# Performance work log

Hardware: AMD Instinct MI355X
Metric: run time of the kernel (lower is better)

The kernel has to match this reference:

```python
import jax, jax.numpy as jnp
import numpy as np

DIM = 1024
HEADS = 16
HEAD_DIM = DIM // HEADS
HIDDEN = 4 * DIM
EPS = 1e-5

def _layernorm(x, w, b):
    mu = jnp.mean(x, axis=-1, keepdims=True)
    var = jnp.mean(jnp.square(x - mu), axis=-1, keepdims=True)
    return (x - mu) * jax.lax.rsqrt(var + EPS) * w + b

def setup_inputs() -> dict:
    key = jax.random.key(0)
    ks = jax.random.split(key, 8)
    B, N, C = 4, 1024, DIM
    s = lambda fan_in: 1.0 / np.sqrt(fan_in)
    return {
        "x": jax.random.normal(ks[0], (B, N, C), dtype=jnp.float32),
        "ln1_w": jnp.ones((C,), jnp.float32),
        "ln1_b": jnp.zeros((C,), jnp.float32),
        "qkv_w": jax.random.normal(ks[1], (3 * C, C), jnp.float32) * s(C),
        "proj_w": jax.random.normal(ks[2], (C, C), jnp.float32) * s(C),
        "proj_b": jnp.zeros((C,), jnp.float32),
        "ln2_w": jnp.ones((C,), jnp.float32),
        "ln2_b": jnp.zeros((C,), jnp.float32),
        "fc1_w": jax.random.normal(ks[3], (HIDDEN, C), jnp.float32) * s(C),
        "fc1_b": jnp.zeros((HIDDEN,), jnp.float32),
        "fc2_w": jax.random.normal(ks[4], (C, HIDDEN), jnp.float32) * s(HIDDEN),
        "fc2_b": jnp.zeros((C,), jnp.float32),
    }

def reference(x, ln1_w, ln1_b, qkv_w, proj_w, proj_b, ln2_w, ln2_b, fc1_w, fc1_b, fc2_w, fc2_b):
    B, N, C = x.shape
    H, D = HEADS, HEAD_DIM
    scale = D ** -0.5
    # --- attention branch (pre-norm) ---
    h = _layernorm(x, ln1_w, ln1_b)
    qkv = jnp.einsum('bnc,oc->bno', h, qkv_w)          # [B,N,3C], no bias (qkv_bias=False)
    qkv = qkv.reshape(B, N, 3, H, D)
    q = jnp.transpose(qkv[:, :, 0], (0, 2, 1, 3))       # [B,H,N,D]
    k = jnp.transpose(qkv[:, :, 1], (0, 2, 1, 3))
    v = jnp.transpose(qkv[:, :, 2], (0, 2, 1, 3))
    attn = jnp.einsum('bhnd,bhmd->bhnm', q, k) * scale  # [B,H,N,N]
    attn = jax.nn.softmax(attn, axis=-1)
    o = jnp.einsum('bhnm,bhmd->bhnd', attn, v)          # [B,H,N,D]
    o = jnp.transpose(o, (0, 2, 1, 3)).reshape(B, N, C)
    o = jnp.einsum('bnc,oc->bno', o, proj_w) + proj_b
    x = x + o
    # --- MLP branch (pre-norm); drop=0.0 -> identity ---
    h = _layernorm(x, ln2_w, ln2_b)
    h = jnp.einsum('bnc,hc->bnh', h, fc1_w) + fc1_b
    h = jax.nn.gelu(h, approximate=False)               # nn.GELU exact erf form
    h = jnp.einsum('bnh,ch->bnc', h, fc2_w) + fc2_b
    return x + h
```

## Files before the change

### kernel.cpp

```cpp
#include <hip/hip_runtime.h>
#include <hip/hip_bf16.h>
#include <math.h>
#include <stdint.h>

#define SEQ 1024
#define CDIM 1024
#define NHEAD 16
#define HIDDEN 4096
#define BATCH 4
#define MROWS (BATCH*SEQ)

using bf16x8 = __attribute__((ext_vector_type(8))) short;
using f32x4  = __attribute__((ext_vector_type(4))) float;

__device__ __forceinline__ short f2bf(float f) {
    union { float f; uint32_t u; } c; c.f = f;
    const uint32_t u = c.u + 0x7FFFu + ((c.u >> 16) & 1u);
    return (short)(u >> 16);
}

__device__ __forceinline__ float gelu_exact(float v) {
    return 0.5f * v * (1.0f + erff(v * 0.70710678118654752440f));
}

__device__ __forceinline__ void gload_lds16(const short* g, short* lds) {
    __builtin_amdgcn_global_load_lds(
        (const __attribute__((address_space(1))) void*)(uintptr_t)g,
        (__attribute__((address_space(3))) void*)(uintptr_t)lds,
        16, 0, 0);
}

__global__ void cvt_bf16_kernel(const float* __restrict__ in, short* __restrict__ out) {
    const size_t i = ((size_t)blockIdx.x * 256 + threadIdx.x) * 8;
    const float4 a = *(const float4*)(in + i);
    const float4 b = *(const float4*)(in + i + 4);
    bf16x8 s;
    s[0] = f2bf(a.x); s[1] = f2bf(a.y); s[2] = f2bf(a.z); s[3] = f2bf(a.w);
    s[4] = f2bf(b.x); s[5] = f2bf(b.y); s[6] = f2bf(b.z); s[7] = f2bf(b.w);
    *(bf16x8*)(out + i) = s;
}

__global__ void ln_kernel(const float* __restrict__ x, const float* __restrict__ w,
                          const float* __restrict__ b, short* __restrict__ out) {
    const int row = blockIdx.x;
    const int t = threadIdx.x;
    const float4* xr = (const float4*)(x + (size_t)row * CDIM);
    float4 v = xr[t];
    float s  = v.x + v.y + v.z + v.w;
    float sq = v.x*v.x + v.y*v.y + v.z*v.z + v.w*v.w;
    #pragma unroll
    for (int off = 32; off; off >>= 1) {
        s  += __shfl_down(s, off);
        sq += __shfl_down(sq, off);
    }
    __shared__ float ss[4], ssq[4];
    const int wid = t >> 6, lane = t & 63;
    if (lane == 0) { ss[wid] = s; ssq[wid] = sq; }
    __syncthreads();
    s  = ss[0] + ss[1] + ss[2] + ss[3];
    sq = ssq[0] + ssq[1] + ssq[2] + ssq[3];
    const float mu  = s * (1.0f / CDIM);
    const float var = sq * (1.0f / CDIM) - mu * mu;
    const float rs  = rsqrtf(var + 1e-5f);
    const float4 wv = ((const float4*)w)[t];
    const float4 bv = ((const float4*)b)[t];
    short4 o;
    o.x = f2bf((v.x - mu) * rs * wv.x + bv.x);
    o.y = f2bf((v.y - mu) * rs * wv.y + bv.y);
    o.z = f2bf((v.z - mu) * rs * wv.z + bv.z);
    o.w = f2bf((v.w - mu) * rs * wv.w + bv.w);
    *(short4*)(out + (size_t)row * CDIM + t * 4) = o;
}

template<int BN, bool BIAS, bool RES, bool GELU_, bool OUTBF16>
__global__ __launch_bounds__(256) void mgemm(
    const short* __restrict__ A, const short* __restrict__ B,
    const float* __restrict__ bias, const float* __restrict__ res,
    void* __restrict__ Cv, int M, int N, int K)
{
    constexpr int MF = (BN == 128) ? 4 : 2;
    __shared__ __align__(16) short As[3][128 * 32];
    __shared__ __align__(16) short Bs[3][BN * 32];
    const int t = threadIdx.x;
    const int w = t >> 6, l = t & 63;

    const int gx = gridDim.x;
    const int nwg = gx * gridDim.y;
    const int lid = blockIdx.y * gx + blockIdx.x;
    const int swz = (lid & 7) * (nwg >> 3) + (lid >> 3);
    const int bx = swz % gx, by = swz / gx;
    const int m0 = by * 128, n0 = bx * BN;

    const int wrow = (BN == 128) ? (w >> 1) * 64 : w * 32;
    const int wcol = (BN == 128) ? (w & 1) * 64 : 0;

    const short* agp0 = A + (size_t)(m0 + w * 32 + (l >> 2)) * K + (l & 3) * 8;
    const short* agp1 = agp0 + (size_t)16 * K;
    const short* bgp0;
    const short* bgp1 = nullptr;
    if (BN == 128) {
        bgp0 = B + (size_t)(n0 + w * 32 + (l >> 2)) * K + (l & 3) * 8;
        bgp1 = bgp0 + (size_t)16 * K;
    } else {
        bgp0 = B + (size_t)(n0 + w * 16 + (l >> 2)) * K + (l & 3) * 8;
    }

    int aoff[MF], boff[4];
    #pragma unroll
    for (int m = 0; m < MF; ++m) aoff[m] = (wrow + m * 16 + (l & 15)) * 32 + (l >> 4) * 8;
    #pragma unroll
    for (int n = 0; n < 4; ++n)  boff[n] = (wcol + n * 16 + (l & 15)) * 32 + (l >> 4) * 8;

    auto stage = [&](int k0, int buf) {
        short* ldsA = &As[buf][w * 1024];
        gload_lds16(agp0 + k0, ldsA);
        gload_lds16(agp1 + k0, ldsA + 512);
        if (BN == 128) {
            short* ldsB = &Bs[buf][w * 1024];
            gload_lds16(bgp0 + k0, ldsB);
            gload_lds16(bgp1 + k0, ldsB + 512);
        } else {
            gload_lds16(bgp0 + k0, &Bs[buf][w * 512]);
        }
    };

    f32x4 acc[MF][4] = {};
    const int T = K / 32;
    stage(0, 0);
    stage(32, 1);
    int cur = 0;
    for (int kt = 0; kt < T; ++kt) {
        if (kt < T - 1) {
            if constexpr (BN == 128) asm volatile("s_waitcnt vmcnt(4)" ::: "memory");
            else                     asm volatile("s_waitcnt vmcnt(3)" ::: "memory");
        } else {
            asm volatile("s_waitcnt vmcnt(0)" ::: "memory");
        }
        __builtin_amdgcn_sched_barrier(0);
        __builtin_amdgcn_s_barrier();
        __builtin_amdgcn_sched_barrier(0);
        if (kt + 2 < T) {
            int nb = kt + 2; nb -= (nb >= 3) ? ((nb / 3) * 3) : 0;
            stage((kt + 2) * 32, nb);
        }
        bf16x8 af[MF], bfr[4];
        #pragma unroll
        for (int m = 0; m < MF; ++m) af[m]  = *(const bf16x8*)&As[cur][aoff[m]];
        #pragma unroll
        for (int n = 0; n < 4; ++n)  bfr[n] = *(const bf16x8*)&Bs[cur][boff[n]];
        #pragma unroll
        for (int m = 0; m < MF; ++m)
            #pragma unroll
            for (int n = 0; n < 4; ++n)
                acc[m][n] = __builtin_amdgcn_mfma_f32_16x16x32_bf16(af[m], bfr[n], acc[m][n], 0, 0, 0);
        cur = (cur == 2) ? 0 : cur + 1;
    }

    const int lr4 = (l >> 4) * 4, lc = l & 15;
    #pragma unroll
    for (int m = 0; m < MF; ++m) {
        #pragma unroll
        for (int n = 0; n < 4; ++n) {
            const int col = n0 + wcol + n * 16 + lc;
            const float bv = BIAS ? bias[col] : 0.0f;
            #pragma unroll
            for (int r = 0; r < 4; ++r) {
                const int row = m0 + wrow + m * 16 + lr4 + r;
                float v = acc[m][n][r] + bv;
                if (GELU_) v = gelu_exact(v);
                if (RES)   v += res[(size_t)row * N + col];
                if (OUTBF16) ((short*)Cv)[(size_t)row * N + col] = f2bf(v);
                else         ((float*)Cv)[(size_t)row * N + col] = v;
            }
        }
    }
}

__global__ __launch_bounds__(256) void qkv_gemm(
    const short* __restrict__ A, const short* __restrict__ B,
    short* __restrict__ qkvb, short* __restrict__ VT, int K)
{
    __shared__ __align__(16) short As[3][128 * 32];
    __shared__ __align__(16) short Bs[3][128 * 32];
    const int t = threadIdx.x;
    const int w = t >> 6, l = t & 63;
    const int wr = w >> 1, wc = w & 1;

    const int gx = gridDim.x;
    const int nwg = gx * gridDim.y;
    const int lid = blockIdx.y * gx + blockIdx.x;
    const int swz = (lid & 7) * (nwg >> 3) + (lid >> 3);
    const int bx = swz % gx, by = swz / gx;
    const int m0 = by * 128, n0 = bx * 128;

    const short* agp0 = A + (size_t)(m0 + w * 32 + (l >> 2)) * K + (l & 3) * 8;
    const short* agp1 = agp0 + (size_t)16 * K;
    const short* bgp0 = B + (size_t)(n0 + w * 32 + (l >> 2)) * K + (l & 3) * 8;
    const short* bgp1 = bgp0 + (size_t)16 * K;

    int aoff[4], boff[4];
    #pragma unroll
    for (int m = 0; m < 4; ++m) aoff[m] = (wr * 64 + m * 16 + (l & 15)) * 32 + (l >> 4) * 8;
    #pragma unroll
    for (int n = 0; n < 4; ++n) boff[n] = (wc * 64 + n * 16 + (l & 15)) * 32 + (l >> 4) * 8;

    auto stage = [&](int k0, int buf) {
        short* ldsA = &As[buf][w * 1024];
        short* ldsB = &Bs[buf][w * 1024];
        gload_lds16(agp0 + k0, ldsA);
        gload_lds16(agp1 + k0, ldsA + 512);
        gload_lds16(bgp0 + k0, ldsB);
        gload_lds16(bgp1 + k0, ldsB + 512);
    };

    f32x4 acc[4][4] = {};
    const int T = K / 32;
    stage(0, 0);
    stage(32, 1);
    int cur = 0;
    for (int kt = 0; kt < T; ++kt) {
        if (kt < T - 1) asm volatile("s_waitcnt vmcnt(4)" ::: "memory");
        else            asm volatile("s_waitcnt vmcnt(0)" ::: "memory");
        __builtin_amdgcn_sched_barrier(0);
        __builtin_amdgcn_s_barrier();
        __builtin_amdgcn_sched_barrier(0);
        if (kt + 2 < T) {
            int nb = kt + 2; nb -= (nb >= 3) ? ((nb / 3) * 3) : 0;
            stage((kt + 2) * 32, nb);
        }
        bf16x8 af[4], bfr[4];
        #pragma unroll
        for (int m = 0; m < 4; ++m) af[m]  = *(const bf16x8*)&As[cur][aoff[m]];
        #pragma unroll
        for (int n = 0; n < 4; ++n) bfr[n] = *(const bf16x8*)&Bs[cur][boff[n]];
        #pragma unroll
        for (int m = 0; m < 4; ++m)
            #pragma unroll
            for (int n = 0; n < 4; ++n)
                acc[m][n] = __builtin_amdgcn_mfma_f32_16x16x32_bf16(af[m], bfr[n], acc[m][n], 0, 0, 0);
        cur = (cur == 2) ? 0 : cur + 1;
    }

    const int lr4 = (l >> 4) * 4, lc = l & 15;
    if (n0 < 2048) {
        const float sc = (n0 < 1024) ? 0.125f : 1.0f;
        #pragma unroll
        for (int m = 0; m < 4; ++m) {
            #pragma unroll
            for (int n = 0; n < 4; ++n) {
                const int col = n0 + wc * 64 + n * 16 + lc;
                #pragma unroll
                for (int r = 0; r < 4; ++r) {
                    const int row = m0 + wr * 64 + m * 16 + lr4 + r;
                    qkvb[(size_t)row * 2048 + col] = f2bf(acc[m][n][r] * sc);
                }
            }
        }
    } else {
        #pragma unroll
        for (int m = 0; m < 4; ++m) {
            const int row0 = m0 + wr * 64 + m * 16 + lr4;
            const int b = row0 >> 10, nseq = row0 & 1023;
            #pragma unroll
            for (int n = 0; n < 4; ++n) {
                const int c2 = n0 - 2048 + wc * 64 + n * 16 + lc;
                const int h = c2 >> 6, d = c2 & 63;
                short4 v4;
                v4.x = f2bf(acc[m][n][0]); v4.y = f2bf(acc[m][n][1]);
                v4.z = f2bf(acc[m][n][2]); v4.w = f2bf(acc[m][n][3]);
                *(short4*)&VT[(((size_t)(b * 16 + h) * 64 + d) * 1024) + nseq] = v4;
            }
        }
    }
}

__global__ __launch_bounds__(256) void fattn(const short* __restrict__ qkvb,
                                             const short* __restrict__ VT,
                                             short* __restrict__ o) {
    const int bh = blockIdx.y;
    const int b = bh >> 4, h = bh & 15;
    const int q0 = blockIdx.x * 64;
    const int t = threadIdx.x, w = t >> 6, l = t & 63;

    __shared__ __align__(16) short Ks[2][64 * 64];
    __shared__ __align__(16) short Vs[2][64 * 64];
    __shared__ __align__(16) short Ps[4][1024];

    const size_t qrow = (size_t)(b * SEQ + q0 + w * 16 + (l & 15)) * 2048 + h * 64;
    bf16x8 qf[2];
    qf[0] = *(const bf16x8*)&qkvb[qrow + (l >> 4) * 8];
    qf[1] = *(const bf16x8*)&qkvb[qrow + 32 + (l >> 4) * 8];

    const int srow = l >> 3;
    const int sc16 = (l & 7) ^ (srow & 7);
    const short* Kg = qkvb + 1024 + h * 64;
    const short* Vg = VT + (size_t)bh * 64 * 1024;

    f32x4 acc[4] = {};
    float mrow[4] = {-1e30f, -1e30f, -1e30f, -1e30f};
    float lrow[4] = {0.f, 0.f, 0.f, 0.f};

    auto stage = [&](int kt, int buf) {
        const int kv0 = kt * 64;
        #pragma unroll
        for (int i = 0; i < 2; ++i) {
            const int r0 = w * 16 + i * 8;
            gload_lds16(Kg + (size_t)(b * SEQ + kv0 + r0 + srow) * 2048 + sc16 * 8,
                        &Ks[buf][r0 * 64]);
            gload_lds16(Vg + (size_t)(r0 + srow) * 1024 + kv0 + sc16 * 8,
                        &Vs[buf][r0 * 64]);
        }
    };

    stage(0, 0);
    for (int kt = 0; kt < 16; ++kt) {
        const int cur = kt & 1;
        __syncthreads();
        if (kt + 1 < 16) stage(kt + 1, cur ^ 1);

        f32x4 sacc[4];
        #pragma unroll
        for (int nt = 0; nt < 4; ++nt) {
            f32x4 z = {};
            #pragma unroll
            for (int ks = 0; ks < 2; ++ks) {
                const int row = nt * 16 + (l & 15);
                const int c16 = (ks * 4 + (l >> 4)) ^ (row & 7);
                const bf16x8 kf = *(const bf16x8*)&Ks[cur][row * 64 + c16 * 8];
                z = __builtin_amdgcn_mfma_f32_16x16x32_bf16(qf[ks], kf, z, 0, 0, 0);
            }
            sacc[nt] = z;
        }
        float tmax[4], tsum[4], fac[4];
        #pragma unroll
        for (int r = 0; r < 4; ++r)
            tmax[r] = fmaxf(fmaxf(sacc[0][r], sacc[1][r]), fmaxf(sacc[2][r], sacc[3][r]));
        #pragma unroll
        for (int off = 1; off <= 8; off <<= 1)
            #pragma unroll
            for (int r = 0; r < 4; ++r)
                tmax[r] = fmaxf(tmax[r], __shfl_xor(tmax[r], off));
        #pragma unroll
        for (int r = 0; r < 4; ++r) {
            const float nm = fmaxf(mrow[r], tmax[r]);
            fac[r] = __expf(mrow[r] - nm);
            mrow[r] = nm;
            tsum[r] = 0.0f;
        }
        #pragma unroll
        for (int nt = 0; nt < 4; ++nt) {
            #pragma unroll
            for (int r = 0; r < 4; ++r) {
                const float p = __expf(sacc[nt][r] - mrow[r]);
                tsum[r] += p;
                const int q = (l >> 4) * 4 + r;
                const int kv = nt * 16 + (l & 15);
                union { float f; uint32_t u; } cu; cu.f = p;
                Ps[w][q * 64 + (kv ^ ((q & 7) << 3))] = (short)((cu.u + 0x8000u) >> 16);
            }
        }
        #pragma unroll
        for (int off = 1; off <= 8; off <<= 1)
            #pragma unroll
            for (int r = 0; r < 4; ++r)
                tsum[r] += __shfl_xor(tsum[r], off);
        #pragma unroll
        for (int r = 0; r < 4; ++r) lrow[r] = lrow[r] * fac[r] + tsum[r];
        #pragma unroll
        for (int nt2 = 0; nt2 < 4; ++nt2)
            #pragma unroll
            for (int r = 0; r < 4; ++r)
                acc[nt2][r] *= fac[r];
        #pragma unroll
        for (int ks = 0; ks < 2; ++ks) {
            const int ql = l & 15;
            const bf16x8 pa = *(const bf16x8*)&Ps[w][ql * 64 + ((ks * 32 + (l >> 4) * 8) ^ ((ql & 7) << 3))];
            #pragma unroll
            for (int nt2 = 0; nt2 < 4; ++nt2) {
                const int row = nt2 * 16 + (l & 15);
                const int c16 = (ks * 4 + (l >> 4)) ^ (row & 7);
                const bf16x8 vf = *(const bf16x8*)&Vs[cur][row * 64 + c16 * 8];
                acc[nt2] = __builtin_amdgcn_mfma_f32_16x16x32_bf16(pa, vf, acc[nt2], 0, 0, 0);
            }
        }
    }
    #pragma unroll
    for (int r = 0; r < 4; ++r) {
        const float rcp = 1.0f / lrow[r];
        const int q = q0 + w * 16 + (l >> 4) * 4 + r;
        #pragma unroll
        for (int nt2 = 0; nt2 < 4; ++nt2) {
            const int d = nt2 * 16 + (l & 15);
            o[(size_t)(b * SEQ + q) * CDIM + h * 64 + d] = f2bf(acc[nt2][r] * rcp);
        }
    }
}

extern "C" void kernel_launch(void* const* d_in, const int* in_sizes, int n_in,
                              void* d_out, int out_size, void* d_ws, size_t ws_size,
                              hipStream_t stream) {
    const float* x      = (const float*)d_in[0];
    const float* ln1_w  = (const float*)d_in[1];
    const float* ln1_b  = (const float*)d_in[2];
    const float* qkv_w  = (const float*)d_in[3];
    const float* proj_w = (const float*)d_in[4];
    const float* proj_b = (const float*)d_in[5];
    const float* ln2_w  = (const float*)d_in[6];
    const float* ln2_b  = (const float*)d_in[7];
    const float* fc1_w  = (const float*)d_in[8];
    const float* fc1_b  = (const float*)d_in[9];
    const float* fc2_w  = (const float*)d_in[10];
    const float* fc2_b  = (const float*)d_in[11];
    float* out = (float*)d_out;

    short* ws16  = (short*)d_ws;
    short* wqkv  = ws16;
    short* wproj = ws16 + 3145728;
    short* wfc1  = ws16 + 4194304;
    short* wfc2  = ws16 + 8388608;
    char*  wsb   = (char*)d_ws;
    short* qkvb  = (short*)(wsb + (size_t)24 * 1024 * 1024);
    short* VT    = (short*)(wsb + (size_t)40 * 1024 * 1024);
    short* mlp1  = (short*)(wsb + (size_t)24 * 1024 * 1024);
    short* hbuf  = (short*)(wsb + (size_t)72 * 1024 * 1024);

    cvt_bf16_kernel<<<1536, 256, 0, stream>>>(qkv_w, wqkv);
    cvt_bf16_kernel<<< 512, 256, 0, stream>>>(proj_w, wproj);
    cvt_bf16_kernel<<<2048, 256, 0, stream>>>(fc1_w, wfc1);
    cvt_bf16_kernel<<<2048, 256, 0, stream>>>(fc2_w, wfc2);

    ln_kernel<<<MROWS, 256, 0, stream>>>(x, ln1_w, ln1_b, hbuf);
    qkv_gemm<<<dim3(24, 32), 256, 0, stream>>>(hbuf, wqkv, qkvb, VT, 1024);
    fattn<<<dim3(SEQ / 64, BATCH * NHEAD), 256, 0, stream>>>(qkvb, VT, hbuf);
    mgemm<64,true,true,false,false><<<dim3(16, 32), 256, 0, stream>>>(
        hbuf, wproj, proj_b, x, out, MROWS, 1024, 1024);
    ln_kernel<<<MROWS, 256, 0, stream>>>(out, ln2_w, ln2_b, hbuf);
    mgemm<128,true,false,true,true><<<dim3(32, 32), 256, 0, stream>>>(
        hbuf, wfc1, fc1_b, nullptr, mlp1, MROWS, 4096, 1024);
    mgemm<64,true,true,false,false><<<dim3(16, 32), 256, 0, stream>>>(
        mlp1, wfc2, fc2_b, out, out, MROWS, 1024, 4096);
}
```

Measured before the change: 252.1 us.

## Swizzle GEMM LDS layout, retile proj/fc2, restructure flash softmax, fuse weight casts

Fuses the four weight-conversion launches into one kernel. Adds an XOR swizzle to the GEMM LDS staging and fragment reads to avoid bank conflicts. Retiles the proj and fc2 GEMMs from 128x64 to 64x128 blocks with a 2x2 wave layout. In attention it swaps the MFMA operands so each lane holds one query row, uses lazy rescaling that skips the max update unless it grows past a threshold, packs P to bf16 with a hardware convert, and remaps blocks so heads share the cache. Several independent changes add risk in correctness and in register pressure.

```diff
diff --git a/kernel.cpp b/kernel.cpp
--- a/kernel.cpp
+++ b/kernel.cpp
@@ -30,8 +30,17 @@
         16, 0, 0);
 }
 
-__global__ void cvt_bf16_kernel(const float* __restrict__ in, short* __restrict__ out) {
-    const size_t i = ((size_t)blockIdx.x * 256 + threadIdx.x) * 8;
+__global__ void cvt_all_kernel(const float* __restrict__ qkv_w, const float* __restrict__ proj_w,
+                               const float* __restrict__ fc1_w, const float* __restrict__ fc2_w,
+                               short* __restrict__ wq, short* __restrict__ wp,
+                               short* __restrict__ w1, short* __restrict__ w2) {
+    const int blk = blockIdx.x;
+    const float* in; short* out; size_t base;
+    if (blk < 1536)      { in = qkv_w;  out = wq; base = (size_t)blk * 2048; }
+    else if (blk < 2048) { in = proj_w; out = wp; base = (size_t)(blk - 1536) * 2048; }
+    else if (blk < 4096) { in = fc1_w;  out = w1; base = (size_t)(blk - 2048) * 2048; }
+    else                 { in = fc2_w;  out = w2; base = (size_t)(blk - 4096) * 2048; }
+    const size_t i = base + (size_t)threadIdx.x * 8;
     const float4 a = *(const float4*)(in + i);
     const float4 b = *(const float4*)(in + i + 4);
     bf16x8 s;
@@ -72,14 +81,17 @@
     *(short4*)(out + (size_t)row * CDIM + t * 4) = o;
 }
 
-template<int BN, bool BIAS, bool RES, bool GELU_, bool OUTBF16>
+template<int BM, int BN, bool BIAS, bool RES, bool GELU_, bool OUTBF16>
 __global__ __launch_bounds__(256) void mgemm(
     const short* __restrict__ A, const short* __restrict__ B,
     const float* __restrict__ bias, const float* __restrict__ res,
     void* __restrict__ Cv, int M, int N, int K)
 {
-    constexpr int MF = (BN == 128) ? 4 : 2;
-    __shared__ __align__(16) short As[3][128 * 32];
+    constexpr int MF = BM / 32;
+    constexpr int NF = BN / 32;
+    constexpr int CA = BM / 64;
+    constexpr int CB = BN / 64;
+    __shared__ __align__(16) short As[3][BM * 32];
     __shared__ __align__(16) short Bs[3][BN * 32];
     const int t = threadIdx.x;
     const int w = t >> 6, l = t & 63;
@@ -87,52 +99,43 @@
     const int gx = gridDim.x;
     const int nwg = gx * gridDim.y;
     const int lid = blockIdx.y * gx + blockIdx.x;
-    const int swz = (lid & 7) * (nwg >> 3) + (lid >> 3);
-    const int bx = swz % gx, by = swz / gx;
-    const int m0 = by * 128, n0 = bx * BN;
-
-    const int wrow = (BN == 128) ? (w >> 1) * 64 : w * 32;
-    const int wcol = (BN == 128) ? (w & 1) * 64 : 0;
-
-    const short* agp0 = A + (size_t)(m0 + w * 32 + (l >> 2)) * K + (l & 3) * 8;
-    const short* agp1 = agp0 + (size_t)16 * K;
-    const short* bgp0;
-    const short* bgp1 = nullptr;
-    if (BN == 128) {
-        bgp0 = B + (size_t)(n0 + w * 32 + (l >> 2)) * K + (l & 3) * 8;
-        bgp1 = bgp0 + (size_t)16 * K;
-    } else {
-        bgp0 = B + (size_t)(n0 + w * 16 + (l >> 2)) * K + (l & 3) * 8;
-    }
-
-    int aoff[MF], boff[4];
-    #pragma unroll
-    for (int m = 0; m < MF; ++m) aoff[m] = (wrow + m * 16 + (l & 15)) * 32 + (l >> 4) * 8;
-    #pragma unroll
-    for (int n = 0; n < 4; ++n)  boff[n] = (wcol + n * 16 + (l & 15)) * 32 + (l >> 4) * 8;
+    const int swzb = (lid & 7) * (nwg >> 3) + (lid >> 3);
+    const int bx = swzb % gx, by = swzb / gx;
+    const int m0 = by * BM, n0 = bx * BN;
+
+    const int wrow = (w >> 1) * (BM / 2);
+    const int wcol = (w & 1) * (BN / 2);
+
+    const int sk8 = ((l & 3) ^ ((l >> 3) & 3)) * 8;
+    const short* agp = A + (size_t)(m0 + w * 16 * CA + (l >> 2)) * K + sk8;
+    const short* bgp = B + (size_t)(n0 + w * 16 * CB + (l >> 2)) * K + sk8;
+
+    const int fr = l & 15;
+    const int rk = ((l >> 4) ^ ((fr >> 1) & 3)) * 8;
+    int aoff[MF], boff[NF];
+    #pragma unroll
+    for (int m = 0; m < MF; ++m) aoff[m] = (wrow + m * 16 + fr) * 32 + rk;
+    #pragma unroll
+    for (int n = 0; n < NF; ++n) boff[n] = (wcol + n * 16 + fr) * 32 + rk;
 
     auto stage = [&](int k0, int buf) {
-        short* ldsA = &As[buf][w * 1024];
-        gload_lds16(agp0 + k0, ldsA);
-        gload_lds16(agp1 + k0, ldsA + 512);
-        if (BN == 128) {
-            short* ldsB = &Bs[buf][w * 1024];
-            gload_lds16(bgp0 + k0, ldsB);
-            gload_lds16(bgp1 + k0, ldsB + 512);
-        } else {
-            gload_lds16(bgp0 + k0, &Bs[buf][w * 512]);
-        }
+        #pragma unroll
+        for (int c = 0; c < CA; ++c)
+            gload_lds16(agp + (size_t)(c * 16) * K + k0, &As[buf][(w * CA + c) * 512]);
+        #pragma unroll
+        for (int c = 0; c < CB; ++c)
+            gload_lds16(bgp + (size_t)(c * 16) * K + k0, &Bs[buf][(w * CB + c) * 512]);
     };
 
-    f32x4 acc[MF][4] = {};
+    f32x4 acc[MF][NF] = {};
     const int T = K / 32;
     stage(0, 0);
     stage(32, 1);
     int cur = 0;
     for (int kt = 0; kt < T; ++kt) {
         if (kt < T - 1) {
-            if constexpr (BN == 128) asm volatile("s_waitcnt vmcnt(4)" ::: "memory");
-            else                     asm volatile("s_waitcnt vmcnt(3)" ::: "memory");
+            if constexpr (CA + CB == 4) asm volatile("s_waitcnt vmcnt(4)" ::: "memory");
+            else                        asm volatile("s_waitcnt vmcnt(3)" ::: "memory");
         } else {
             asm volatile("s_waitcnt vmcnt(0)" ::: "memory");
         }
@@ -143,15 +146,15 @@
             int nb = kt + 2; nb -= (nb >= 3) ? ((nb / 3) * 3) : 0;
             stage((kt + 2) * 32, nb);
         }
-        bf16x8 af[MF], bfr[4];
+        bf16x8 af[MF], bfr[NF];
         #pragma unroll
         for (int m = 0; m < MF; ++m) af[m]  = *(const bf16x8*)&As[cur][aoff[m]];
         #pragma unroll
-        for (int n = 0; n < 4; ++n)  bfr[n] = *(const bf16x8*)&Bs[cur][boff[n]];
+        for (int n = 0; n < NF; ++n) bfr[n] = *(const bf16x8*)&Bs[cur][boff[n]];
         #pragma unroll
         for (int m = 0; m < MF; ++m)
             #pragma unroll
-            for (int n = 0; n < 4; ++n)
+            for (int n = 0; n < NF; ++n)
                 acc[m][n] = __builtin_amdgcn_mfma_f32_16x16x32_bf16(af[m], bfr[n], acc[m][n], 0, 0, 0);
         cur = (cur == 2) ? 0 : cur + 1;
     }
@@ -160,7 +163,7 @@
     #pragma unroll
     for (int m = 0; m < MF; ++m) {
         #pragma unroll
-        for (int n = 0; n < 4; ++n) {
+        for (int n = 0; n < NF; ++n) {
             const int col = n0 + wcol + n * 16 + lc;
             const float bv = BIAS ? bias[col] : 0.0f;
             #pragma unroll
@@ -176,7 +179,7 @@
     }
 }
 
-__global__ __launch_bounds__(256) void qkv_gemm(
+__global__ __launch_bounds__(256) void qkv_m(
     const short* __restrict__ A, const short* __restrict__ B,
     short* __restrict__ qkvb, short* __restrict__ VT, int K)
 {
@@ -184,33 +187,36 @@
     __shared__ __align__(16) short Bs[3][128 * 32];
     const int t = threadIdx.x;
     const int w = t >> 6, l = t & 63;
-    const int wr = w >> 1, wc = w & 1;
 
     const int gx = gridDim.x;
     const int nwg = gx * gridDim.y;
     const int lid = blockIdx.y * gx + blockIdx.x;
-    const int swz = (lid & 7) * (nwg >> 3) + (lid >> 3);
-    const int bx = swz % gx, by = swz / gx;
+    const int swzb = (lid & 7) * (nwg >> 3) + (lid >> 3);
+    const int bx = swzb % gx, by = swzb / gx;
     const int m0 = by * 128, n0 = bx * 128;
 
-    const short* agp0 = A + (size_t)(m0 + w * 32 + (l >> 2)) * K + (l & 3) * 8;
-    const short* agp1 = agp0 + (size_t)16 * K;
-    const short* bgp0 = B + (size_t)(n0 + w * 32 + (l >> 2)) * K + (l & 3) * 8;
-    const short* bgp1 = bgp0 + (size_t)16 * K;
-
+    const int wrow = (w >> 1) * 64;
+    const int wcol = (w & 1) * 64;
+
+    const int sk8 = ((l & 3) ^ ((l >> 3) & 3)) * 8;
+    const short* agp = A + (size_t)(m0 + w * 32 + (l >> 2)) * K + sk8;
+    const short* bgp = B + (size_t)(n0 + w * 32 + (l >> 2)) * K + sk8;
+
+    const int fr = l & 15;
+    const int rk = ((l >> 4) ^ ((fr >> 1) & 3)) * 8;
     int aoff[4], boff[4];
     #pragma unroll
-    for (int m = 0; m < 4; ++m) aoff[m] = (wr * 64 + m * 16 + (l & 15)) * 32 + (l >> 4) * 8;
-    #pragma unroll
-    for (int n = 0; n < 4; ++n) boff[n] = (wc * 64 + n * 16 + (l & 15)) * 32 + (l >> 4) * 8;
+    for (int m = 0; m < 4; ++m) aoff[m] = (wrow + m * 16 + fr) * 32 + rk;
+    #pragma unroll
+    for (int n = 0; n < 4; ++n) boff[n] = (wcol + n * 16 + fr) * 32 + rk;
 
     auto stage = [&](int k0, int buf) {
-        short* ldsA = &As[buf][w * 1024];
-        short* ldsB = &Bs[buf][w * 1024];
-        gload_lds16(agp0 + k0, ldsA);
-        gload_lds16(agp1 + k0, ldsA + 512);
-        gload_lds16(bgp0 + k0, ldsB);
-        gload_lds16(bgp1 + k0, ldsB + 512);
+        #pragma unroll
+        for (int c = 0; c < 2; ++c)
+            gload_lds16(agp + (size_t)(c * 16) * K + k0, &As[buf][(w * 2 + c) * 512]);
+        #pragma unroll
+        for (int c = 0; c < 2; ++c)
+            gload_lds16(bgp + (size_t)(c * 16) * K + k0, &Bs[buf][(w * 2 + c) * 512]);
     };
 
     f32x4 acc[4][4] = {};
@@ -248,10 +254,10 @@
         for (int m = 0; m < 4; ++m) {
             #pragma unroll
             for (int n = 0; n < 4; ++n) {
-                const int col = n0 + wc * 64 + n * 16 + lc;
+                const int col = n0 + wcol + n * 16 + lc;
                 #pragma unroll
                 for (int r = 0; r < 4; ++r) {
-                    const int row = m0 + wr * 64 + m * 16 + lr4 + r;
+                    const int row = m0 + wrow + m * 16 + lr4 + r;
                     qkvb[(size_t)row * 2048 + col] = f2bf(acc[m][n][r] * sc);
                 }
             }
@@ -259,11 +265,11 @@
     } else {
         #pragma unroll
         for (int m = 0; m < 4; ++m) {
-            const int row0 = m0 + wr * 64 + m * 16 + lr4;
+            const int row0 = m0 + wrow + m * 16 + lr4;
             const int b = row0 >> 10, nseq = row0 & 1023;
             #pragma unroll
             for (int n = 0; n < 4; ++n) {
-                const int c2 = n0 - 2048 + wc * 64 + n * 16 + lc;
+                const int c2 = n0 - 2048 + wcol + n * 16 + lc;
                 const int h = c2 >> 6, d = c2 & 63;
                 short4 v4;
                 v4.x = f2bf(acc[m][n][0]); v4.y = f2bf(acc[m][n][1]);
@@ -277,9 +283,10 @@
 __global__ __launch_bounds__(256) void fattn(const short* __restrict__ qkvb,
                                              const short* __restrict__ VT,
                                              short* __restrict__ o) {
-    const int bh = blockIdx.y;
+    const int lid = blockIdx.y * gridDim.x + blockIdx.x;
+    const int bh = ((lid >> 7) << 3) | (lid & 7);
+    const int q0 = ((lid >> 3) & 15) * 64;
     const int b = bh >> 4, h = bh & 15;
-    const int q0 = blockIdx.x * 64;
     const int t = threadIdx.x, w = t >> 6, l = t & 63;
 
     __shared__ __align__(16) short Ks[2][64 * 64];
@@ -297,8 +304,9 @@
     const short* Vg = VT + (size_t)bh * 64 * 1024;
 
     f32x4 acc[4] = {};
-    float mrow[4] = {-1e30f, -1e30f, -1e30f, -1e30f};
-    float lrow[4] = {0.f, 0.f, 0.f, 0.f};
+    float mr = -1e30f, lr = 0.0f;
+    const int q = l & 15;
+    const int g4 = (l >> 4) & 3;
 
     auto stage = [&](int kt, int buf) {
         const int kv0 = kt * 64;
@@ -327,50 +335,57 @@
                 const int row = nt * 16 + (l & 15);
                 const int c16 = (ks * 4 + (l >> 4)) ^ (row & 7);
                 const bf16x8 kf = *(const bf16x8*)&Ks[cur][row * 64 + c16 * 8];
-                z = __builtin_amdgcn_mfma_f32_16x16x32_bf16(qf[ks], kf, z, 0, 0, 0);
+                z = __builtin_amdgcn_mfma_f32_16x16x32_bf16(kf, qf[ks], z, 0, 0, 0);
             }
             sacc[nt] = z;
         }
-        float tmax[4], tsum[4], fac[4];
-        #pragma unroll
-        for (int r = 0; r < 4; ++r)
-            tmax[r] = fmaxf(fmaxf(sacc[0][r], sacc[1][r]), fmaxf(sacc[2][r], sacc[3][r]));
-        #pragma unroll
-        for (int off = 1; off <= 8; off <<= 1)
+        float tm = sacc[0][0];
+        #pragma unroll
+        for (int nt = 0; nt < 4; ++nt)
+            #pragma unroll
+            for (int r = 0; r < 4; ++r) tm = fmaxf(tm, sacc[nt][r]);
+        tm = fmaxf(tm, __shfl_xor(tm, 16));
+        tm = fmaxf(tm, __shfl_xor(tm, 32));
+        const bool norescale = __all(tm <= mr + 8.0f);
+        float fac = 1.0f;
+        if (!norescale) {
+            const float nm = fmaxf(mr, tm);
+            fac = __expf(mr - nm);
+            mr = nm;
+        }
+        float p[4][4];
+        float ts = 0.0f;
+        #pragma unroll
+        for (int nt = 0; nt < 4; ++nt)
+            #pragma unroll
+            for (int r = 0; r < 4; ++r) {
+                p[nt][r] = __expf(sacc[nt][r] - mr);
+                ts += p[nt][r];
+            }
+        ts += __shfl_xor(ts, 16);
+        ts += __shfl_xor(ts, 32);
+        lr = lr * fac + ts;
+        if (!norescale) {
+            float facv[4];
             #pragma unroll
             for (int r = 0; r < 4; ++r)
-                tmax[r] = fmaxf(tmax[r], __shfl_xor(tmax[r], off));
-        #pragma unroll
-        for (int r = 0; r < 4; ++r) {
-            const float nm = fmaxf(mrow[r], tmax[r]);
-            fac[r] = __expf(mrow[r] - nm);
-            mrow[r] = nm;
-            tsum[r] = 0.0f;
+                facv[r] = __shfl(fac, (l & 48) + g4 * 4 + r);
+            #pragma unroll
+            for (int nt2 = 0; nt2 < 4; ++nt2)
+                #pragma unroll
+                for (int r = 0; r < 4; ++r)
+                    acc[nt2][r] *= facv[r];
         }
         #pragma unroll
         for (int nt = 0; nt < 4; ++nt) {
-            #pragma unroll
-            for (int r = 0; r < 4; ++r) {
-                const float p = __expf(sacc[nt][r] - mrow[r]);
-                tsum[r] += p;
-                const int q = (l >> 4) * 4 + r;
-                const int kv = nt * 16 + (l & 15);
-                union { float f; uint32_t u; } cu; cu.f = p;
-                Ps[w][q * 64 + (kv ^ ((q & 7) << 3))] = (short)((cu.u + 0x8000u) >> 16);
-            }
-        }
-        #pragma unroll
-        for (int off = 1; off <= 8; off <<= 1)
-            #pragma unroll
-            for (int r = 0; r < 4; ++r)
-                tsum[r] += __shfl_xor(tsum[r], off);
-        #pragma unroll
-        for (int r = 0; r < 4; ++r) lrow[r] = lrow[r] * fac[r] + tsum[r];
-        #pragma unroll
-        for (int nt2 = 0; nt2 < 4; ++nt2)
-            #pragma unroll
-            for (int r = 0; r < 4; ++r)
-                acc[nt2][r] *= fac[r];
+            uint32_t lo, hi;
+            asm("v_cvt_pk_bf16_f32 %0, %1, %2" : "=v"(lo) : "v"(p[nt][0]), "v"(p[nt][1]));
+            asm("v_cvt_pk_bf16_f32 %0, %1, %2" : "=v"(hi) : "v"(p[nt][2]), "v"(p[nt][3]));
+            const int kvb = nt * 16 + g4 * 4;
+            const int addr = q * 64 + (((kvb >> 3) ^ (q & 7)) << 3) + (kvb & 7);
+            *(uint2*)&Ps[w][addr] = make_uint2(lo, hi);
+        }
+        asm volatile("s_waitcnt lgkmcnt(0)" ::: "memory");
         #pragma unroll
         for (int ks = 0; ks < 2; ++ks) {
             const int ql = l & 15;
@@ -384,14 +399,15 @@
             }
         }
     }
+    float rcpl = 1.0f / lr;
     #pragma unroll
     for (int r = 0; r < 4; ++r) {
-        const float rcp = 1.0f / lrow[r];
-        const int q = q0 + w * 16 + (l >> 4) * 4 + r;
+        const float rcp = __shfl(rcpl, (l & 48) + g4 * 4 + r);
+        const int qq = q0 + w * 16 + g4 * 4 + r;
         #pragma unroll
         for (int nt2 = 0; nt2 < 4; ++nt2) {
             const int d = nt2 * 16 + (l & 15);
-            o[(size_t)(b * SEQ + q) * CDIM + h * 64 + d] = f2bf(acc[nt2][r] * rcp);
+            o[(size_t)(b * SEQ + qq) * CDIM + h * 64 + d] = f2bf(acc[nt2][r] * rcp);
         }
     }
 }
@@ -424,19 +440,17 @@
     short* mlp1  = (short*)(wsb + (size_t)24 * 1024 * 1024);
     short* hbuf  = (short*)(wsb + (size_t)72 * 1024 * 1024);
 
-    cvt_bf16_kernel<<<1536, 256, 0, stream>>>(qkv_w, wqkv);
-    cvt_bf16_kernel<<< 512, 256, 0, stream>>>(proj_w, wproj);
-    cvt_bf16_kernel<<<2048, 256, 0, stream>>>(fc1_w, wfc1);
-    cvt_bf16_kernel<<<2048, 256, 0, stream>>>(fc2_w, wfc2);
+    cvt_all_kernel<<<6144, 256, 0, stream>>>(qkv_w, proj_w, fc1_w, fc2_w,
+                                             wqkv, wproj, wfc1, wfc2);
 
     ln_kernel<<<MROWS, 256, 0, stream>>>(x, ln1_w, ln1_b, hbuf);
-    qkv_gemm<<<dim3(24, 32), 256, 0, stream>>>(hbuf, wqkv, qkvb, VT, 1024);
-    fattn<<<dim3(SEQ / 64, BATCH * NHEAD), 256, 0, stream>>>(qkvb, VT, hbuf);
-    mgemm<64,true,true,false,false><<<dim3(16, 32), 256, 0, stream>>>(
+    qkv_m<<<dim3(24, 32), 256, 0, stream>>>(hbuf, wqkv, qkvb, VT, 1024);
+    fattn<<<dim3(16, 64), 256, 0, stream>>>(qkvb, VT, hbuf);
+    mgemm<64,128,true,true,false,false><<<dim3(8, 64), 256, 0, stream>>>(
         hbuf, wproj, proj_b, x, out, MROWS, 1024, 1024);
     ln_kernel<<<MROWS, 256, 0, stream>>>(out, ln2_w, ln2_b, hbuf);
-    mgemm<128,true,false,true,true><<<dim3(32, 32), 256, 0, stream>>>(
+    mgemm<128,128,true,false,true,true><<<dim3(32, 32), 256, 0, stream>>>(
         hbuf, wfc1, fc1_b, nullptr, mlp1, MROWS, 4096, 1024);
-    mgemm<64,true,true,false,false><<<dim3(16, 32), 256, 0, stream>>>(
+    mgemm<64,128,true,true,false,false><<<dim3(8, 64), 256, 0, stream>>>(
         mlp1, wfc2, fc2_b, out, out, MROWS, 1024, 4096);
 }
```

After: 227.9 us. -9.6%, faster.
